# Kernel optimization log

Measured on AMD Instinct MI355X. Metric: run time of the kernel, lower is better.

Reference implementation:

```python
import jax, jax.numpy as jnp
import numpy as np

B, S, IN, D, H, K, NLVL = 8, 1536, 32, 128, 4, 7, 2
DFF = 4 * D
DK = D // H
EPS = 1e-6


def setup_inputs() -> dict:
    key = jax.random.key(0)
    ks = jax.random.split(key, 24)
    rn = lambda k, sh, s=0.05: jax.random.normal(k, sh, jnp.float32) * s
    z = lambda sh: jnp.zeros(sh, jnp.float32)
    o = lambda sh: jnp.ones(sh, jnp.float32)
    return {
        'x': jax.random.normal(ks[0], (B, S, IN), jnp.float32),
        'enc_W': rn(ks[1], (IN, D)), 'enc_b': z((D,)),
        'ln_rnn_a': o((NLVL, D)), 'ln_rnn_b': z((NLVL, D)),
        'gru_Wih': rn(ks[2], (NLVL, 3 * D, D)), 'gru_Whh': rn(ks[3], (NLVL, 3 * D, D)),
        'gru_bih': z((NLVL, 3 * D)), 'gru_bhh': z((NLVL, 3 * D)),
        'ln_attn_a': o((NLVL, D)), 'ln_attn_b': z((NLVL, D)),
        'Wq': rn(ks[4], (NLVL, D, D)), 'bq': z((NLVL, D)),
        'Wk': rn(ks[5], (NLVL, D, D)), 'bk': z((NLVL, D)),
        'Wv': rn(ks[6], (NLVL, D, D)), 'bv': z((NLVL, D)),
        'Wo': rn(ks[7], (NLVL, D, D)), 'bo': z((NLVL, D)),
        'ln_ff_a': o((NLVL, D)), 'ln_ff_b': z((NLVL, D)),
        'ff_W1': rn(ks[8], (NLVL, D, DFF)), 'ff_b1': z((NLVL, DFF)),
        'ff_W2': rn(ks[9], (NLVL, DFF, D)), 'ff_b2': z((NLVL, D)),
        'out_W': rn(ks[10], (D, 1)), 'out_b': z((1,)),
    }


def layernorm(x, a, b):
    # faithful to torch code: unbiased std (ddof=1), divide by (std + eps)
    m = x.mean(-1, keepdims=True)
    s = jnp.std(x, axis=-1, ddof=1, keepdims=True)
    return a * (x - m) / (s + EPS) + b


def local_rnn(x, Wih, Whh, bih, bhh):
    # x: [B,S,D]. Window each position into its ksize-length causal window,
    # run a GRU over the window (scan over K steps, batched over B*S), keep last h.
    xp = jnp.pad(x, ((0, 0), (K - 1, 0), (0, 0)))            # zero left-pad
    win = jnp.stack([xp[:, i:i + S] for i in range(K)], 0)   # [K,B,S,D]

    def step(h, xt):
        gi = xt @ Wih.T + bih                                 # [B,S,3D]
        gh = h @ Whh.T + bhh
        ir, iz, inn = jnp.split(gi, 3, -1)
        hr, hz, hn = jnp.split(gh, 3, -1)
        r = jax.nn.sigmoid(ir + hr)
        zz = jax.nn.sigmoid(iz + hz)
        nn_ = jnp.tanh(inn + r * hn)
        return (1.0 - zz) * nn_ + zz * h, None

    h, _ = jax.lax.scan(step, jnp.zeros_like(x), win)
    return h


def mhpool(x, Wq, bq, Wk, bk, Wv, bv, Wo, bo):
    def heads(w, bb):
        return jnp.swapaxes((x @ w + bb).reshape(B, S, H, DK), 1, 2)  # [B,H,S,DK]
    q, k, v = heads(Wq, bq), heads(Wk, bk), heads(Wv, bv)
    scores = jnp.einsum('bhqd,bhkd->bhqk', q, k) / np.float32(np.sqrt(DK))
    mask = jnp.tril(jnp.ones((S, S), bool))
    scores = jnp.where(mask, scores, jnp.float32(-1e9))
    p = jax.nn.softmax(scores, axis=-1)
    o = jnp.einsum('bhqk,bhkd->bhqd', p, v)
    o = jnp.swapaxes(o, 1, 2).reshape(B, S, D)
    return o @ Wo + bo


def reference(x, enc_W, enc_b, ln_rnn_a, ln_rnn_b, gru_Wih, gru_Whh, gru_bih,
              gru_bhh, ln_attn_a, ln_attn_b, Wq, bq, Wk, bk, Wv, bv, Wo, bo,
              ln_ff_a, ln_ff_b, ff_W1, ff_b1, ff_W2, ff_b2, out_W, out_b):
    h = x @ enc_W + enc_b
    for i in range(NLVL):
        # LocalRNNLayer (pre-norm residual); LocalRNN.output Linear is unused in orig forward
        h = h + local_rnn(layernorm(h, ln_rnn_a[i], ln_rnn_b[i]),
                          gru_Wih[i], gru_Whh[i], gru_bih[i], gru_bhh[i])
        # MHPooling sublayer
        h = h + mhpool(layernorm(h, ln_attn_a[i], ln_attn_b[i]),
                       Wq[i], bq[i], Wk[i], bk[i], Wv[i], bv[i], Wo[i], bo[i])
        # PositionwiseFeedForward sublayer
        hn = layernorm(h, ln_ff_a[i], ln_ff_b[i])
        h = h + (jax.nn.relu(hn @ ff_W1[i] + ff_b1[i]) @ ff_W2[i] + ff_b2[i])
    return jax.nn.sigmoid(h @ out_W + out_b)
```

## Files before the change

kernel.cpp:

```cpp
#include <hip/hip_runtime.h>
#include <math.h>

#define DEV_INLINE __device__ __forceinline__

constexpr int B = 8, S = 1536, IN = 32, D = 128, NH = 4, KWIN = 7, NLVL = 2;
constexpr int DFF = 512, DKH = 32;
constexpr int M = B * S;
constexpr int MD = M * D;
constexpr float EPS = 1e-6f;

typedef unsigned short u16;
typedef __bf16 bf16x8 __attribute__((ext_vector_type(8)));
typedef float f32x4 __attribute__((ext_vector_type(4)));
typedef unsigned short u16x4 __attribute__((ext_vector_type(4)));

#define MFMA16(a, b, c) __builtin_amdgcn_mfma_f32_16x16x32_bf16(a, b, c, 0, 0, 0)

DEV_INLINE float sigmoidf_(float x) { return 1.f / (1.f + __expf(-x)); }

DEV_INLINE u16 f2bf(float f) {
    unsigned u = __builtin_bit_cast(unsigned, f);
    unsigned rnd = 0x7FFFu + ((u >> 16) & 1u);
    return (u16)((u + rnd) >> 16);
}
// ... 59 lines not shown
        if (i < SZ_FF) {
            int lvl = i >> 16, rem = i & 65535, k = rem >> 7, n = rem & 127;
            W2T[(size_t)lvl * 65536 + n * 512 + k] = f2bf(W2[i]); return;
        }
        return;
    }
    const int row0 = (blockIdx.x - 2304) * 32;
    for (int i = tid; i < 32 * 32; i += 256) xs[i >> 5][i & 31] = x[(size_t)row0 * IN + i];
    for (int i = tid; i < 32 * 128; i += 256) Ws[i >> 7][i & 127] = encW[i];
    __syncthreads();
    const int r = tid >> 3, cg = (tid & 7) * 16;
    float acc[16];
    #pragma unroll
    for (int j = 0; j < 16; ++j) acc[j] = encb[cg + j];
    for (int k = 0; k < IN; ++k) {
        const float xv = xs[r][k];
        #pragma unroll
        for (int j = 0; j < 16; ++j) acc[j] = fmaf(xv, Ws[k][cg + j], acc[j]);
    }
    float s = 0.f;
    #pragma unroll
    for (int j = 0; j < 16; ++j) s += acc[j];
    s += __shfl_xor(s, 1); s += __shfl_xor(s, 2); s += __shfl_xor(s, 4);
    const float mean = s * (1.f / D);
    float q = 0.f;
    #pragma unroll
    for (int j = 0; j < 16; ++j) { float d = acc[j] - mean; q += d * d; }
    q += __shfl_xor(q, 1); q += __shfl_xor(q, 2); q += __shfl_xor(q, 4);
    const float inv = 1.f / (sqrtf(q * (1.f / (D - 1))) + EPS);
    float* hp = h + (size_t)(row0 + r) * D + cg;
    u16* xp = xnout + (size_t)(row0 + r) * D + cg;
    #pragma unroll
    for (int jj = 0; jj < 4; ++jj) {
        float4 hv = make_float4(acc[4 * jj], acc[4 * jj + 1], acc[4 * jj + 2], acc[4 * jj + 3]);
        *(float4*)(hp + 4 * jj) = hv;
        u16x4 o;
        #pragma unroll
        for (int c = 0; c < 4; ++c)
            o[c] = f2bf(ga[cg + 4 * jj + c] * (acc[4 * jj + c] - mean) * inv + gb[cg + 4 * jj + c]);
        *(u16x4*)(xp + 4 * jj) = o;
    }
}

__global__ __launch_bounds__(512, 2) void k_gru_qkv(
    const u16* __restrict__ xn,
    const u16* __restrict__ Wih16,
    const u16* __restrict__ Whh16,
    const float* __restrict__ bih, const float* __restrict__ bhh,
    float* __restrict__ hout,
    const float* __restrict__ ga, const float* __restrict__ gb,
    const u16* __restrict__ Wqkv,
    const float* __restrict__ bq, const float* __restrict__ bk, const float* __restrict__ bv,
    u16* __restrict__ q16, u16* __restrict__ k16, u16* __restrict__ vt16) {
    constexpr int RB = 48;
    constexpr float QS = 0.17677669529663687f * 1.4426950408889634f;
    __shared__ __align__(16) u16 xnS[64 * 136];
    __shared__ __align__(16) u16 Gs[64 * 392];
    __shared__ __align__(16) u16 hs16[RB * 136];
    const int tid = threadIdx.x;
    const int wave = tid >> 6, lane = tid & 63;
    const int col16 = lane & 15, quad = lane >> 4;
    const int row0 = blockIdx.x * RB;
    const int ss0 = row0 % S;
    const int cc = wave * 16 + col16;

    for (int i = tid; i < 64 * 16; i += 512) {
        const int r = i >> 4, c8 = (i & 15) * 8;
        bf16x8 val = {};
        if (ss0 - 16 + r >= 0)
            val = *(const bf16x8*)(xn + (size_t)(row0 - 16 + r) * 128 + c8);
        *(bf16x8*)&xnS[r * 136 + c8] = val;
    }
    bf16x8 Breg[3][4];
    #pragma unroll
    for (int g = 0; g < 3; ++g)
        #pragma unroll
        for (int kc = 0; kc < 4; ++kc)
            Breg[g][kc] = *(const bf16x8*)(Whh16 + (size_t)(g * 128 + cc) * 128 + kc * 32 + quad * 8);
    float bi[3], bh[3];
    #pragma unroll
    for (int g = 0; g < 3; ++g) { bi[g] = bih[g * 128 + cc]; bh[g] = bhh[g * 128 + cc]; }
    __syncthreads();

    #pragma unroll
    for (int tt = wave; tt < 24; tt += 8) {
        const int rt = tt / 12, ct = tt - rt * 12;
        const u16* bp = Wih16 + (size_t)(ct * 32 + col16) * 128 + quad * 8;
        f32x4 a00 = {0.f, 0.f, 0.f, 0.f}, a01 = a00, a10 = a00, a11 = a00;
        #pragma unroll
        for (int k0 = 0; k0 < 128; k0 += 32) {
            bf16x8 af0 = *(const bf16x8*)&xnS[(rt * 32 + col16) * 136 + k0 + quad * 8];
            bf16x8 af1 = *(const bf16x8*)&xnS[(rt * 32 + 16 + col16) * 136 + k0 + quad * 8];
            bf16x8 b0 = *(const bf16x8*)(bp + k0);
            bf16x8 b1 = *(const bf16x8*)(bp + 16 * 128 + k0);
            a00 = MFMA16(af0, b0, a00);
            a01 = MFMA16(af0, b1, a01);
            a10 = MFMA16(af1, b0, a10);
            a11 = MFMA16(af1, b1, a11);
        }
        #pragma unroll
        for (int r = 0; r < 4; ++r) {
            const int gr0 = rt * 32 + quad * 4 + r, gr1 = gr0 + 16;
            Gs[gr0 * 392 + ct * 32 + col16]      = f2bf(a00[r]);
            Gs[gr0 * 392 + ct * 32 + 16 + col16] = f2bf(a01[r]);
            Gs[gr1 * 392 + ct * 32 + col16]      = f2bf(a10[r]);
            Gs[gr1 * 392 + ct * 32 + 16 + col16] = f2bf(a11[r]);
        }
    }
    float hp[12] = {};
    __syncthreads();

    for (int t = 0; t < KWIN; ++t) {
        const int shift = KWIN - 1 - t;
        f32x4 acc[3][3];
        #pragma unroll
        for (int rh = 0; rh < 3; ++rh)
            #pragma unroll
            for (int g = 0; g < 3; ++g) acc[rh][g] = {0.f, 0.f, 0.f, 0.f};
        if (t > 0) {
            bf16x8 af[3][4];
            #pragma unroll
            for (int rh = 0; rh < 3; ++rh)
                #pragma unroll
                for (int kc = 0; kc < 4; ++kc)
                    af[rh][kc] = *(const bf16x8*)&hs16[(rh * 16 + col16) * 136 + kc * 32 + quad * 8];
            __syncthreads();
            #pragma unroll
            for (int kc = 0; kc < 4; ++kc)
                #pragma unroll
                for (int g = 0; g < 3; ++g)
                    #pragma unroll
                    for (int rh = 0; rh < 3; ++rh)
                        acc[rh][g] = MFMA16(af[rh][kc], Breg[g][kc], acc[rh][g]);
        }
        const bool last = (t == KWIN - 1);
        #pragma unroll
        for (int rh = 0; rh < 3; ++rh) {
            #pragma unroll
            for (int r = 0; r < 4; ++r) {
                const int idx = rh * 4 + r;
                const int lrow = rh * 16 + quad * 4 + r;
                const int gr = lrow - shift + 16;
                const float xr  = b2f(Gs[gr * 392 + cc]);
                const float xz  = b2f(Gs[gr * 392 + 128 + cc]);
                const float xn_ = b2f(Gs[gr * 392 + 256 + cc]);
                const float rr = sigmoidf_(xr + bi[0] + acc[rh][0][r] + bh[0]);
                const float zz = sigmoidf_(xz + bi[1] + acc[rh][1][r] + bh[1]);
                const float e2 = __expf(2.f * (xn_ + bi[2] + rr * (acc[rh][2][r] + bh[2])));
                const float nn = 1.f - 2.f / (e2 + 1.f);
                const float hnew = (1.f - zz) * nn + zz * hp[idx];
                hp[idx] = hnew;
                if (!last) hs16[lrow * 136 + cc] = f2bf(hnew);
            }
        }
        __syncthreads();
    }
    float* hf = (float*)Gs;
    #pragma unroll
    for (int rh = 0; rh < 3; ++rh)
        #pragma unroll
        for (int r = 0; r < 4; ++r) {
            const int lrow = rh * 16 + quad * 4 + r;
            const float hv = hp[rh * 4 + r] + hout[(size_t)(row0 + lrow) * D + cc];
            hout[(size_t)(row0 + lrow) * D + cc] = hv;
            hf[lrow * 132 + cc] = hv;
        }
    __syncthreads();
    {
        const int r = tid >> 3;
        if (r < RB) {
            const int cg = (tid & 7) * 16;
            float vals[16];
            #pragma unroll
            for (int jj = 0; jj < 4; ++jj) {
                float4 v = *(const float4*)&hf[r * 132 + cg + 4 * jj];
                vals[4 * jj] = v.x; vals[4 * jj + 1] = v.y; vals[4 * jj + 2] = v.z; vals[4 * jj + 3] = v.w;
            }
            float s = 0.f;
            #pragma unroll
            for (int j = 0; j < 16; ++j) s += vals[j];
            s += __shfl_xor(s, 1); s += __shfl_xor(s, 2); s += __shfl_xor(s, 4);
            const float mean = s * (1.f / D);
            float q = 0.f;
            #pragma unroll
            for (int j = 0; j < 16; ++j) { float d = vals[j] - mean; q += d * d; }
            q += __shfl_xor(q, 1); q += __shfl_xor(q, 2); q += __shfl_xor(q, 4);
            const float inv = 1.f / (sqrtf(q * (1.f / (D - 1))) + EPS);
            #pragma unroll
            for (int jj = 0; jj < 4; ++jj) {
                u16x4 o;
                #pragma unroll
                for (int c = 0; c < 4; ++c)
                    o[c] = f2bf(ga[cg + 4 * jj + c] * (vals[4 * jj + c] - mean) * inv + gb[cg + 4 * jj + c]);
                *(u16x4*)&hs16[r * 136 + cg + 4 * jj] = o;
            }
        }
    }
    __syncthreads();
    for (int tt = wave; tt < 36; tt += 8) {
        const int rt = tt / 12, ct = tt - rt * 12;
        const int seg = ct >> 2;
        const int c0 = (ct & 3) * 32;
        const u16* bp = Wqkv + (size_t)(seg * 128 + c0 + col16) * 128 + quad * 8;
        f32x4 a0 = {0.f, 0.f, 0.f, 0.f}, a1 = a0;
        #pragma unroll
        for (int k0 = 0; k0 < 128; k0 += 32) {
            bf16x8 af = *(const bf16x8*)&hs16[(rt * 16 + col16) * 136 + k0 + quad * 8];
            bf16x8 b0 = *(const bf16x8*)(bp + k0);
            bf16x8 b1 = *(const bf16x8*)(bp + 16 * 128 + k0);
            a0 = MFMA16(af, b0, a0);
            a1 = MFMA16(af, b1, a1);
        }
        if (seg < 2) {
            const float* bias = seg == 0 ? bq : bk;
            const float sc = seg == 0 ? QS : 1.f;
            const float bv0 = bias[c0 + col16], bv1 = bias[c0 + 16 + col16];
            u16* o16 = seg == 0 ? q16 : k16;
            #pragma unroll
            for (int r = 0; r < 4; ++r) {
                const size_t gr = (size_t)(row0 + rt * 16 + quad * 4 + r) * 128;
                o16[gr + c0 + col16]      = f2bf((a0[r] + bv0) * sc);
                o16[gr + c0 + 16 + col16] = f2bf((a1[r] + bv1) * sc);
            }
        } else {
            const float bv0 = bv[c0 + col16], bv1 = bv[c0 + 16 + col16];
            const int bb = row0 / S, ssv = row0 - bb * S + rt * 16;
            const int ca = c0 + col16, cb = c0 + 16 + col16;
            u16* pa = vt16 + ((size_t)((bb * NH + (ca >> 5)) * 32 + (ca & 31))) * S + ssv;
            u16* pb = vt16 + ((size_t)((bb * NH + (cb >> 5)) * 32 + (cb & 31))) * S + ssv;
            #pragma unroll
            for (int r = 0; r < 4; ++r) {
                pa[quad * 4 + r] = f2bf(a0[r] + bv0);
                pb[quad * 4 + r] = f2bf(a1[r] + bv1);
            }
        }
    }
}

__global__ __launch_bounds__(256) void k_attn_mfma(
    const u16* Qb, const u16* __restrict__ Kb,
    const u16* __restrict__ Vt, u16* O16) {
    const int wave = threadIdx.x >> 6, lane = threadIdx.x & 63;
    const int p = blockIdx.x;
    const int bh = blockIdx.y;
    const int b = bh >> 2, hh = bh & 3;
    const int col = lane & 15, quad = lane >> 4;

    __shared__ __align__(16) u16 Pb[4][32][40];
    __shared__ float Om[4][32][33];
    __shared__ float Lm[4][32];
    u16 (* __restrict__ P)[40] = Pb[wave];

    const u16* Kbase = Kb + (size_t)b * S * 128 + hh * 32;
    const u16* Vbase = Vt + (size_t)bh * 32 * S;

    #pragma unroll
    for (int half = 0; half < 2; ++half) {
        const int qt = half == 0 ? p : 47 - p;
        const int q0 = qt * 32;
        const int nkt = qt + 1;
        const u16* qp = Qb + (size_t)(b * S + q0 + col) * 128 + hh * 32 + quad * 8;
        const bf16x8 qf0 = *(const bf16x8*)qp;
        const bf16x8 qf1 = *(const bf16x8*)(qp + 16 * 128);
        f32x4 o00 = {0.f, 0.f, 0.f, 0.f}, o01 = o00, o10 = o00, o11 = o00;
        float lsum[8] = {};
        int kt = wave;
        bf16x8 kf0 = {}, kf1 = {}, vf0 = {}, vf1 = {};
        if (kt < nkt) {
            const u16* kp = Kbase + (size_t)(kt * 32 + col) * 128 + quad * 8;
            kf0 = *(const bf16x8*)kp;
            kf1 = *(const bf16x8*)(kp + 16 * 128);
            const u16* vp = Vbase + (size_t)col * S + kt * 32 + quad * 8;
            vf0 = *(const bf16x8*)vp;
            vf1 = *(const bf16x8*)(vp + 16 * S);
        }
        while (kt < nkt) {
            const int ktn = kt + 4;
            bf16x8 nk0 = kf0, nk1 = kf1, nv0 = vf0, nv1 = vf1;
            if (ktn < nkt) {
                const u16* kp = Kbase + (size_t)(ktn * 32 + col) * 128 + quad * 8;
                nk0 = *(const bf16x8*)kp;
                nk1 = *(const bf16x8*)(kp + 16 * 128);
                const u16* vp = Vbase + (size_t)col * S + ktn * 32 + quad * 8;
                nv0 = *(const bf16x8*)vp;
                nv1 = *(const bf16x8*)(vp + 16 * S);
            }
// ... 30 lines not shown
            o00 = MFMA16(pa0, vf0, o00);
            o01 = MFMA16(pa0, vf1, o01);
            o10 = MFMA16(pa1, vf0, o10);
            o11 = MFMA16(pa1, vf1, o11);
            kf0 = nk0; kf1 = nk1; vf0 = nv0; vf1 = nv1;
            kt = ktn;
        }
        #pragma unroll
        for (int i = 0; i < 8; ++i) {
            float v = lsum[i];
            v += __shfl_xor(v, 1); v += __shfl_xor(v, 2);
            v += __shfl_xor(v, 4); v += __shfl_xor(v, 8);
            lsum[i] = v;
        }
        #pragma unroll
        for (int r = 0; r < 4; ++r) {
            const int lr = quad * 4 + r;
            Om[wave][lr][col]           = o00[r];
            Om[wave][lr][16 + col]      = o01[r];
            Om[wave][16 + lr][col]      = o10[r];
            Om[wave][16 + lr][16 + col] = o11[r];
        }
        if (col == 0) {
            #pragma unroll
            for (int i = 0; i < 8; ++i)
                Lm[wave][(i >> 2) * 16 + quad * 4 + (i & 3)] = lsum[i];
        }
        __syncthreads();
        {
            const int tr = threadIdx.x >> 3, tc = (threadIdx.x & 7) * 4;
            const float inv = 1.f / (Lm[0][tr] + Lm[1][tr] + Lm[2][tr] + Lm[3][tr]);
            u16x4 outv;
            #pragma unroll
            for (int c = 0; c < 4; ++c) {
                const float o = Om[0][tr][tc + c] + Om[1][tr][tc + c] +
                                Om[2][tr][tc + c] + Om[3][tr][tc + c];
                outv[c] = f2bf(o * inv);
            }
            *(u16x4*)(O16 + (size_t)(b * S + q0 + tr) * 128 + hh * 32 + tc) = outv;
        }
        __syncthreads();
    }
}

template <bool LAST>
__global__ __launch_bounds__(256) void k_mho_ffn(
    const u16* __restrict__ ao, const u16* __restrict__ WoT, const float* __restrict__ bo,
    float* __restrict__ hio,
    const float* __restrict__ ga1, const float* __restrict__ gb1,
    const u16* __restrict__ W1T, const float* __restrict__ b1,
    const u16* __restrict__ W2T, const float* __restrict__ b2,
    const float* __restrict__ ga2, const float* __restrict__ gb2, u16* __restrict__ xnout,
    const float* __restrict__ outW, const float* __restrict__ outb, float* __restrict__ outp) {
    __shared__ float hL[32 * 132];
    __shared__ __align__(16) u16 xnL[32 * 136];
    __shared__ __align__(16) u16 Ls[32 * 520];
    const int tid = threadIdx.x;
    const int wave = tid >> 6, lane = tid & 63;
    const int col16 = lane & 15, quad = lane >> 4;
    const int row0 = blockIdx.x * 32;
    const int c0 = wave * 32;

    {
        const u16* a0p = ao + (size_t)(row0 + col16) * 128 + quad * 8;
        const u16* b0p = WoT + (size_t)(c0 + col16) * 128 + quad * 8;
        f32x4 acc00 = {0.f, 0.f, 0.f, 0.f}, acc01 = acc00, acc10 = acc00, acc11 = acc00;
        mfma_tile32<128>(a0p, a0p + 16 * 128, b0p, b0p + 16 * 128, acc00, acc01, acc10, acc11);
        const float bv0 = bo[c0 + col16];
        const float bv1 = bo[c0 + 16 + col16];
        #pragma unroll
        for (int r = 0; r < 4; ++r) {
            const int l0 = quad * 4 + r, l1 = 16 + quad * 4 + r;
            const size_t g0 = (size_t)(row0 + l0) * D, g1 = (size_t)(row0 + l1) * D;
            hL[l0 * 132 + c0 + col16]      = acc00[r] + bv0 + hio[g0 + c0 + col16];
            hL[l0 * 132 + c0 + 16 + col16] = acc01[r] + bv1 + hio[g0 + c0 + 16 + col16];
            hL[l1 * 132 + c0 + col16]      = acc10[r] + bv0 + hio[g1 + c0 + col16];
            hL[l1 * 132 + c0 + 16 + col16] = acc11[r] + bv1 + hio[g1 + c0 + 16 + col16];
        }
    }
    __syncthreads();
    {
        const int r = tid >> 3, cg = (tid & 7) * 16;
        float vals[16];
        #pragma unroll
        for (int jj = 0; jj < 4; ++jj) {
            float4 v = *(const float4*)&hL[r * 132 + cg + 4 * jj];
            vals[4 * jj] = v.x; vals[4 * jj + 1] = v.y; vals[4 * jj + 2] = v.z; vals[4 * jj + 3] = v.w;
        }
        float s = 0.f;
        #pragma unroll
        for (int j = 0; j < 16; ++j) s += vals[j];
        s += __shfl_xor(s, 1); s += __shfl_xor(s, 2); s += __shfl_xor(s, 4);
        const float mean = s * (1.f / D);
        float q = 0.f;
        #pragma unroll
        for (int j = 0; j < 16; ++j) { float d = vals[j] - mean; q += d * d; }
        q += __shfl_xor(q, 1); q += __shfl_xor(q, 2); q += __shfl_xor(q, 4);
        const float inv = 1.f / (sqrtf(q * (1.f / (D - 1))) + EPS);
        #pragma unroll
        for (int jj = 0; jj < 4; ++jj) {
            u16x4 o;
            #pragma unroll
            for (int c = 0; c < 4; ++c)
                o[c] = f2bf(ga1[cg + 4 * jj + c] * (vals[4 * jj + c] - mean) * inv + gb1[cg + 4 * jj + c]);
            *(u16x4*)&xnL[r * 136 + cg + 4 * jj] = o;
        }
    }
    __syncthreads();
    #pragma unroll
    for (int ct = 0; ct < 4; ++ct) {
        const int c0f = wave * 128 + ct * 32;
        const u16* b0p = W1T + (size_t)(c0f + col16) * 128 + quad * 8;
        f32x4 acc00 = {0.f, 0.f, 0.f, 0.f}, acc01 = acc00, acc10 = acc00, acc11 = acc00;
        #pragma unroll
        for (int k0 = 0; k0 < 128; k0 += 32) {
            bf16x8 a0 = *(const bf16x8*)&xnL[col16 * 136 + k0 + quad * 8];
            bf16x8 a1 = *(const bf16x8*)&xnL[(16 + col16) * 136 + k0 + quad * 8];
            bf16x8 b0 = *(const bf16x8*)(b0p + k0);
            bf16x8 b1 = *(const bf16x8*)(b0p + 16 * 128 + k0);
            acc00 = MFMA16(a0, b0, acc00);
            acc01 = MFMA16(a0, b1, acc01);
            acc10 = MFMA16(a1, b0, acc10);
            acc11 = MFMA16(a1, b1, acc11);
        }
        const float bv0 = b1[c0f + col16];
        const float bv1 = b1[c0f + 16 + col16];
        #pragma unroll
        for (int r = 0; r < 4; ++r) {
            const int l0 = quad * 4 + r, l1 = 16 + quad * 4 + r;
            Ls[l0 * 520 + c0f + col16]      = f2bf(fmaxf(acc00[r] + bv0, 0.f));
            Ls[l0 * 520 + c0f + 16 + col16] = f2bf(fmaxf(acc01[r] + bv1, 0.f));
            Ls[l1 * 520 + c0f + col16]      = f2bf(fmaxf(acc10[r] + bv0, 0.f));
            Ls[l1 * 520 + c0f + 16 + col16] = f2bf(fmaxf(acc11[r] + bv1, 0.f));
        }
    }
    __syncthreads();
    {
        f32x4 acc00 = {0.f, 0.f, 0.f, 0.f}, acc01 = acc00, acc10 = acc00, acc11 = acc00;
        #pragma unroll
        for (int k0 = 0; k0 < 512; k0 += 32) {
            bf16x8 a0 = *(const bf16x8*)&Ls[col16 * 520 + k0 + quad * 8];
            bf16x8 a1 = *(const bf16x8*)&Ls[(16 + col16) * 520 + k0 + quad * 8];
            const u16* bp = W2T + (size_t)(c0 + col16) * 512 + k0 + quad * 8;
            bf16x8 b0 = *(const bf16x8*)bp;
            bf16x8 b1v = *(const bf16x8*)(bp + 16 * 512);
            acc00 = MFMA16(a0, b0, acc00);
            acc01 = MFMA16(a0, b1v, acc01);
            acc10 = MFMA16(a1, b0, acc10);
            acc11 = MFMA16(a1, b1v, acc11);
        }
        const float bv0 = b2[c0 + col16];
        const float bv1 = b2[c0 + 16 + col16];
        #pragma unroll
        for (int r = 0; r < 4; ++r) {
            const int l0 = quad * 4 + r, l1 = 16 + quad * 4 + r;
            const size_t g0 = (size_t)(row0 + l0) * D, g1 = (size_t)(row0 + l1) * D;
            const float v00 = acc00[r] + bv0 + hL[l0 * 132 + c0 + col16];
            const float v01 = acc01[r] + bv1 + hL[l0 * 132 + c0 + 16 + col16];
            const float v10 = acc10[r] + bv0 + hL[l1 * 132 + c0 + col16];
            const float v11 = acc11[r] + bv1 + hL[l1 * 132 + c0 + 16 + col16];
            hio[g0 + c0 + col16]      = v00;
            hio[g0 + c0 + 16 + col16] = v01;
            hio[g1 + c0 + col16]      = v10;
            hio[g1 + c0 + 16 + col16] = v11;
            hL[l0 * 132 + c0 + col16]      = v00;
            hL[l0 * 132 + c0 + 16 + col16] = v01;
            hL[l1 * 132 + c0 + col16]      = v10;
            hL[l1 * 132 + c0 + 16 + col16] = v11;
        }
    }
    __syncthreads();
    {
        const int r = tid >> 3, cg = (tid & 7) * 16;
        float vals[16];
        #pragma unroll
        for (int jj = 0; jj < 4; ++jj) {
            float4 v = *(const float4*)&hL[r * 132 + cg + 4 * jj];
            vals[4 * jj] = v.x; vals[4 * jj + 1] = v.y; vals[4 * jj + 2] = v.z; vals[4 * jj + 3] = v.w;
        }
        if constexpr (LAST) {
            float dot = 0.f;
            #pragma unroll
            for (int j = 0; j < 16; ++j) dot += vals[j] * outW[cg + j];
            dot += __shfl_xor(dot, 1); dot += __shfl_xor(dot, 2); dot += __shfl_xor(dot, 4);
            if ((tid & 7) == 0) outp[row0 + r] = sigmoidf_(dot + outb[0]);
        } else {
            float s = 0.f;
            #pragma unroll
            for (int j = 0; j < 16; ++j) s += vals[j];
            s += __shfl_xor(s, 1); s += __shfl_xor(s, 2); s += __shfl_xor(s, 4);
            const float mean = s * (1.f / D);
            float q = 0.f;
            #pragma unroll
            for (int j = 0; j < 16; ++j) { float d = vals[j] - mean; q += d * d; }
            q += __shfl_xor(q, 1); q += __shfl_xor(q, 2); q += __shfl_xor(q, 4);
            const float inv = 1.f / (sqrtf(q * (1.f / (D - 1))) + EPS);
            u16* xp = xnout + (size_t)(row0 + r) * D + cg;
            #pragma unroll
            for (int jj = 0; jj < 4; ++jj) {
                u16x4 o;
                #pragma unroll
                for (int c = 0; c < 4; ++c)
                    o[c] = f2bf(ga2[cg + 4 * jj + c] * (vals[4 * jj + c] - mean) * inv + gb2[cg + 4 * jj + c]);
                *(u16x4*)(xp + 4 * jj) = o;
            }
        }
    }
}

extern "C" void kernel_launch(void* const* d_in, const int* in_sizes, int n_in,
                              void* d_out, int out_size, void* d_ws, size_t ws_size,
                              hipStream_t stream) {
    const float* x       = (const float*)d_in[0];
    const float* enc_W   = (const float*)d_in[1];
    const float* enc_b   = (const float*)d_in[2];
    const float* ln_rnn_a = (const float*)d_in[3];
    const float* ln_rnn_b = (const float*)d_in[4];
    const float* gru_Wih = (const float*)d_in[5];
    const float* gru_Whh = (const float*)d_in[6];
    const float* gru_bih = (const float*)d_in[7];
    const float* gru_bhh = (const float*)d_in[8];
    const float* ln_attn_a = (const float*)d_in[9];
    const float* ln_attn_b = (const float*)d_in[10];
    const float* Wq = (const float*)d_in[11];
    const float* bq = (const float*)d_in[12];
    const float* Wk = (const float*)d_in[13];
    const float* bk = (const float*)d_in[14];
    const float* Wv = (const float*)d_in[15];
    const float* bv = (const float*)d_in[16];
    const float* Wo = (const float*)d_in[17];
    const float* bo = (const float*)d_in[18];
    const float* ln_ff_a = (const float*)d_in[19];
    const float* ln_ff_b = (const float*)d_in[20];
    const float* ff_W1 = (const float*)d_in[21];
    const float* ff_b1 = (const float*)d_in[22];
    const float* ff_W2 = (const float*)d_in[23];
    const float* ff_b2 = (const float*)d_in[24];
    const float* out_W = (const float*)d_in[25];
    const float* out_b = (const float*)d_in[26];

    float* h   = (float*)d_ws;
    u16* pool  = (u16*)(h + MD);
    u16* xn16  = pool + (size_t)3 * MD;
    u16* Wih16 = xn16 + MD;
    u16* Whh16 = Wih16 + NLVL * 384 * D;
    u16* Wqkv  = Whh16 + NLVL * 384 * D;
    u16* WoT   = Wqkv + NLVL * 384 * D;
    u16* W1T   = WoT + NLVL * D * D;
    u16* W2T   = W1T + NLVL * D * DFF;

    u16* q16   = pool;
    u16* k16   = pool + MD;
    u16* vt16  = pool + (size_t)2 * MD;
    u16* ao16  = q16;

    k_prep_enc<<<2688, 256, 0, stream>>>(
        gru_Wih, gru_Whh, Wq, Wk, Wv, Wo, ff_W1, ff_W2,
        Wih16, Whh16, Wqkv, WoT, W1T, W2T,
        x, enc_W, enc_b, ln_rnn_a, ln_rnn_b, h, xn16);

    for (int lvl = 0; lvl < NLVL; ++lvl) {
        k_gru_qkv<<<256, 512, 0, stream>>>(
            xn16, Wih16 + lvl * 384 * D, Whh16 + lvl * 384 * D,
            gru_bih + lvl * 384, gru_bhh + lvl * 384,
            h, ln_attn_a + lvl * D, ln_attn_b + lvl * D,
            Wqkv + lvl * 384 * D, bq + lvl * D, bk + lvl * D, bv + lvl * D,
            q16, k16, vt16);

        k_attn_mfma<<<dim3(24, 32), 256, 0, stream>>>(q16, k16, vt16, ao16);

        if (lvl + 1 < NLVL) {
            k_mho_ffn<false><<<M / 32, 256, 0, stream>>>(
                ao16, WoT + lvl * D * D, bo + lvl * D, h,
                ln_ff_a + lvl * D, ln_ff_b + lvl * D,
                W1T + lvl * D * DFF, ff_b1 + lvl * DFF,
                W2T + lvl * DFF * D, ff_b2 + lvl * D,
                ln_rnn_a + (lvl + 1) * D, ln_rnn_b + (lvl + 1) * D, xn16,
                nullptr, nullptr, nullptr);
        } else {
            k_mho_ffn<true><<<M / 32, 256, 0, stream>>>(
                ao16, WoT + lvl * D * D, bo + lvl * D, h,
                ln_ff_a + lvl * D, ln_ff_b + lvl * D,
                W1T + lvl * D * DFF, ff_b1 + lvl * DFF,
                W2T + lvl * DFF * D, ff_b2 + lvl * D,
                nullptr, nullptr, nullptr,
                out_W, out_b, (float*)d_out);
        }
    }
}
```

Measured before the change: 320.0 us.

## Double-buffer GRU hidden state, trim halo, load x from global, halve FFN row tile

The GRU kernel no longer stages the normalized input in shared memory. The input projection reads its A operand directly from global, and the window halo shrinks from 16 rows to 6, so Gs shrinks to 54 rows. The hidden-state buffer is double-buffered, which removes one __syncthreads per recurrence step. Separately, the MHO/FFN kernel processes 16 rows per block instead of 32, doubling the grid and cutting shared memory and registers for occupancy, at the cost of reloading weights twice as often.

```diff
diff --git a/kernel.cpp b/kernel.cpp
--- a/kernel.cpp
+++ b/kernel.cpp
@@ -137,9 +137,9 @@
     u16* __restrict__ q16, u16* __restrict__ k16, u16* __restrict__ vt16) {
     constexpr int RB = 48;
     constexpr float QS = 0.17677669529663687f * 1.4426950408889634f;
-    __shared__ __align__(16) u16 xnS[64 * 136];
-    __shared__ __align__(16) u16 Gs[64 * 392];
-    __shared__ __align__(16) u16 hs16[RB * 136];
+    __shared__ __align__(16) u16 Gs[54 * 392];
+    __shared__ __align__(16) u16 hsA[RB * 136];
+    __shared__ __align__(16) u16 hsB[RB * 136];
     const int tid = threadIdx.x;
     const int wave = tid >> 6, lane = tid & 63;
     const int col16 = lane & 15, quad = lane >> 4;
@@ -147,13 +147,6 @@
     const int ss0 = row0 % S;
     const int cc = wave * 16 + col16;
 
-    for (int i = tid; i < 64 * 16; i += 512) {
-        const int r = i >> 4, c8 = (i & 15) * 8;
-        bf16x8 val = {};
-        if (ss0 - 16 + r >= 0)
-            val = *(const bf16x8*)(xn + (size_t)(row0 - 16 + r) * 128 + c8);
-        *(bf16x8*)&xnS[r * 136 + c8] = val;
-    }
     bf16x8 Breg[3][4];
     #pragma unroll
     for (int g = 0; g < 3; ++g)
@@ -163,17 +156,23 @@
     float bi[3], bh[3];
     #pragma unroll
     for (int g = 0; g < 3; ++g) { bi[g] = bih[g * 128 + cc]; bh[g] = bhh[g * 128 + cc]; }
-    __syncthreads();
 
     #pragma unroll
     for (int tt = wave; tt < 24; tt += 8) {
         const int rt = tt / 12, ct = tt - rt * 12;
+        const int gr0 = rt * 22;
+        const bool v0 = (ss0 - 6 + gr0 + col16) >= 0;
+        const int grow0 = row0 - 6 + gr0 + col16;
+        const int grow1 = grow0 + 16;
+        const u16* a0g = xn + (size_t)(v0 ? grow0 : row0) * 128 + quad * 8;
+        const u16* a1g = xn + (size_t)grow1 * 128 + quad * 8;
         const u16* bp = Wih16 + (size_t)(ct * 32 + col16) * 128 + quad * 8;
         f32x4 a00 = {0.f, 0.f, 0.f, 0.f}, a01 = a00, a10 = a00, a11 = a00;
         #pragma unroll
         for (int k0 = 0; k0 < 128; k0 += 32) {
-            bf16x8 af0 = *(const bf16x8*)&xnS[(rt * 32 + col16) * 136 + k0 + quad * 8];
-            bf16x8 af1 = *(const bf16x8*)&xnS[(rt * 32 + 16 + col16) * 136 + k0 + quad * 8];
+            bf16x8 af0 = *(const bf16x8*)(a0g + k0);
+            if (!v0) af0 = (bf16x8){};
+            bf16x8 af1 = *(const bf16x8*)(a1g + k0);
             bf16x8 b0 = *(const bf16x8*)(bp + k0);
             bf16x8 b1 = *(const bf16x8*)(bp + 16 * 128 + k0);
             a00 = MFMA16(af0, b0, a00);
@@ -183,11 +182,11 @@
         }
         #pragma unroll
         for (int r = 0; r < 4; ++r) {
-            const int gr0 = rt * 32 + quad * 4 + r, gr1 = gr0 + 16;
-            Gs[gr0 * 392 + ct * 32 + col16]      = f2bf(a00[r]);
-            Gs[gr0 * 392 + ct * 32 + 16 + col16] = f2bf(a01[r]);
-            Gs[gr1 * 392 + ct * 32 + col16]      = f2bf(a10[r]);
-            Gs[gr1 * 392 + ct * 32 + 16 + col16] = f2bf(a11[r]);
+            const int g0r = gr0 + quad * 4 + r, g1r = g0r + 16;
+            Gs[g0r * 392 + ct * 32 + col16]      = f2bf(a00[r]);
+            Gs[g0r * 392 + ct * 32 + 16 + col16] = f2bf(a01[r]);
+            Gs[g1r * 392 + ct * 32 + col16]      = f2bf(a10[r]);
+            Gs[g1r * 392 + ct * 32 + 16 + col16] = f2bf(a11[r]);
         }
     }
     float hp[12] = {};
@@ -195,6 +194,8 @@
 
     for (int t = 0; t < KWIN; ++t) {
         const int shift = KWIN - 1 - t;
+        u16* wbuf = (t & 1) ? hsB : hsA;
+        const u16* rbuf = (t & 1) ? hsA : hsB;
         f32x4 acc[3][3];
         #pragma unroll
         for (int rh = 0; rh < 3; ++rh)
@@ -206,8 +207,7 @@
             for (int rh = 0; rh < 3; ++rh)
                 #pragma unroll
                 for (int kc = 0; kc < 4; ++kc)
-                    af[rh][kc] = *(const bf16x8*)&hs16[(rh * 16 + col16) * 136 + kc * 32 + quad * 8];
-            __syncthreads();
+                    af[rh][kc] = *(const bf16x8*)&rbuf[(rh * 16 + col16) * 136 + kc * 32 + quad * 8];
             #pragma unroll
             for (int kc = 0; kc < 4; ++kc)
                 #pragma unroll
@@ -223,7 +223,7 @@
             for (int r = 0; r < 4; ++r) {
                 const int idx = rh * 4 + r;
                 const int lrow = rh * 16 + quad * 4 + r;
-                const int gr = lrow - shift + 16;
+                const int gr = lrow - shift + 6;
                 const float xr  = b2f(Gs[gr * 392 + cc]);
                 const float xz  = b2f(Gs[gr * 392 + 128 + cc]);
                 const float xn_ = b2f(Gs[gr * 392 + 256 + cc]);
@@ -233,7 +233,7 @@
                 const float nn = 1.f - 2.f / (e2 + 1.f);
                 const float hnew = (1.f - zz) * nn + zz * hp[idx];
                 hp[idx] = hnew;
-                if (!last) hs16[lrow * 136 + cc] = f2bf(hnew);
+                if (!last) wbuf[lrow * 136 + cc] = f2bf(hnew);
             }
         }
         __syncthreads();
@@ -275,7 +275,7 @@
                 #pragma unroll
                 for (int c = 0; c < 4; ++c)
                     o[c] = f2bf(ga[cg + 4 * jj + c] * (vals[4 * jj + c] - mean) * inv + gb[cg + 4 * jj + c]);
-                *(u16x4*)&hs16[r * 136 + cg + 4 * jj] = o;
+                *(u16x4*)&hsA[r * 136 + cg + 4 * jj] = o;
             }
         }
     }
@@ -288,7 +288,7 @@
         f32x4 a0 = {0.f, 0.f, 0.f, 0.f}, a1 = a0;
         #pragma unroll
         for (int k0 = 0; k0 < 128; k0 += 32) {
-            bf16x8 af = *(const bf16x8*)&hs16[(rt * 16 + col16) * 136 + k0 + quad * 8];
+            bf16x8 af = *(const bf16x8*)&hsA[(rt * 16 + col16) * 136 + k0 + quad * 8];
             bf16x8 b0 = *(const bf16x8*)(bp + k0);
             bf16x8 b1 = *(const bf16x8*)(bp + 16 * 128 + k0);
             a0 = MFMA16(af, b0, a0);
@@ -451,53 +451,58 @@
     const u16* __restrict__ W2T, const float* __restrict__ b2,
     const float* __restrict__ ga2, const float* __restrict__ gb2, u16* __restrict__ xnout,
     const float* __restrict__ outW, const float* __restrict__ outb, float* __restrict__ outp) {
-    __shared__ float hL[32 * 132];
-    __shared__ __align__(16) u16 xnL[32 * 136];
-    __shared__ __align__(16) u16 Ls[32 * 520];
+    __shared__ float hL[16 * 132];
+    __shared__ __align__(16) u16 xnL[16 * 136];
+    __shared__ __align__(16) u16 Ls[16 * 520];
     const int tid = threadIdx.x;
     const int wave = tid >> 6, lane = tid & 63;
     const int col16 = lane & 15, quad = lane >> 4;
-    const int row0 = blockIdx.x * 32;
+    const int row0 = blockIdx.x * 16;
     const int c0 = wave * 32;
 
     {
         const u16* a0p = ao + (size_t)(row0 + col16) * 128 + quad * 8;
         const u16* b0p = WoT + (size_t)(c0 + col16) * 128 + quad * 8;
-        f32x4 acc00 = {0.f, 0.f, 0.f, 0.f}, acc01 = acc00, acc10 = acc00, acc11 = acc00;
-        mfma_tile32<128>(a0p, a0p + 16 * 128, b0p, b0p + 16 * 128, acc00, acc01, acc10, acc11);
-        const float bv0 = bo[c0 + col16];
-        const float bv1 = bo[c0 + 16 + col16];
+        const u16* b1p = b0p + 16 * 128;
+        f32x4 acc0 = {0.f, 0.f, 0.f, 0.f}, acc1 = acc0;
+        #pragma unroll
+        for (int k0 = 0; k0 < 128; k0 += 32) {
+            bf16x8 a0 = *(const bf16x8*)(a0p + k0);
+            bf16x8 b0 = *(const bf16x8*)(b0p + k0);
+            bf16x8 b1 = *(const bf16x8*)(b1p + k0);
+            acc0 = MFMA16(a0, b0, acc0);
+            acc1 = MFMA16(a0, b1, acc1);
+        }
+        const float bv0 = bo[c0 + col16], bv1 = bo[c0 + 16 + col16];
         #pragma unroll
         for (int r = 0; r < 4; ++r) {
-            const int l0 = quad * 4 + r, l1 = 16 + quad * 4 + r;
-            const size_t g0 = (size_t)(row0 + l0) * D, g1 = (size_t)(row0 + l1) * D;
-            hL[l0 * 132 + c0 + col16]      = acc00[r] + bv0 + hio[g0 + c0 + col16];
-            hL[l0 * 132 + c0 + 16 + col16] = acc01[r] + bv1 + hio[g0 + c0 + 16 + col16];
-            hL[l1 * 132 + c0 + col16]      = acc10[r] + bv0 + hio[g1 + c0 + col16];
-            hL[l1 * 132 + c0 + 16 + col16] = acc11[r] + bv1 + hio[g1 + c0 + 16 + col16];
+            const int l0 = quad * 4 + r;
+            const size_t g0 = (size_t)(row0 + l0) * D;
+            hL[l0 * 132 + c0 + col16]      = acc0[r] + bv0 + hio[g0 + c0 + col16];
+            hL[l0 * 132 + c0 + 16 + col16] = acc1[r] + bv1 + hio[g0 + c0 + 16 + col16];
         }
     }
     __syncthreads();
     {
-        const int r = tid >> 3, cg = (tid & 7) * 16;
-        float vals[16];
-        #pragma unroll
-        for (int jj = 0; jj < 4; ++jj) {
+        const int r = tid >> 4, cg = (tid & 15) * 8;
+        float vals[8];
+        #pragma unroll
+        for (int jj = 0; jj < 2; ++jj) {
             float4 v = *(const float4*)&hL[r * 132 + cg + 4 * jj];
             vals[4 * jj] = v.x; vals[4 * jj + 1] = v.y; vals[4 * jj + 2] = v.z; vals[4 * jj + 3] = v.w;
         }
         float s = 0.f;
         #pragma unroll
-        for (int j = 0; j < 16; ++j) s += vals[j];
-        s += __shfl_xor(s, 1); s += __shfl_xor(s, 2); s += __shfl_xor(s, 4);
+        for (int j = 0; j < 8; ++j) s += vals[j];
+        s += __shfl_xor(s, 1); s += __shfl_xor(s, 2); s += __shfl_xor(s, 4); s += __shfl_xor(s, 8);
         const float mean = s * (1.f / D);
         float q = 0.f;
         #pragma unroll
-        for (int j = 0; j < 16; ++j) { float d = vals[j] - mean; q += d * d; }
-        q += __shfl_xor(q, 1); q += __shfl_xor(q, 2); q += __shfl_xor(q, 4);
+        for (int j = 0; j < 8; ++j) { float d = vals[j] - mean; q += d * d; }
+        q += __shfl_xor(q, 1); q += __shfl_xor(q, 2); q += __shfl_xor(q, 4); q += __shfl_xor(q, 8);
         const float inv = 1.f / (sqrtf(q * (1.f / (D - 1))) + EPS);
         #pragma unroll
-        for (int jj = 0; jj < 4; ++jj) {
+        for (int jj = 0; jj < 2; ++jj) {
             u16x4 o;
             #pragma unroll
             for (int c = 0; c < 4; ++c)
@@ -510,93 +515,79 @@
     for (int ct = 0; ct < 4; ++ct) {
         const int c0f = wave * 128 + ct * 32;
         const u16* b0p = W1T + (size_t)(c0f + col16) * 128 + quad * 8;
-        f32x4 acc00 = {0.f, 0.f, 0.f, 0.f}, acc01 = acc00, acc10 = acc00, acc11 = acc00;
+        const u16* b1p = b0p + 16 * 128;
+        f32x4 acc0 = {0.f, 0.f, 0.f, 0.f}, acc1 = acc0;
         #pragma unroll
         for (int k0 = 0; k0 < 128; k0 += 32) {
             bf16x8 a0 = *(const bf16x8*)&xnL[col16 * 136 + k0 + quad * 8];
-            bf16x8 a1 = *(const bf16x8*)&xnL[(16 + col16) * 136 + k0 + quad * 8];
             bf16x8 b0 = *(const bf16x8*)(b0p + k0);
-            bf16x8 b1 = *(const bf16x8*)(b0p + 16 * 128 + k0);
-            acc00 = MFMA16(a0, b0, acc00);
-            acc01 = MFMA16(a0, b1, acc01);
-            acc10 = MFMA16(a1, b0, acc10);
-            acc11 = MFMA16(a1, b1, acc11);
-        }
-        const float bv0 = b1[c0f + col16];
-        const float bv1 = b1[c0f + 16 + col16];
+            bf16x8 b1 = *(const bf16x8*)(b1p + k0);
+            acc0 = MFMA16(a0, b0, acc0);
+            acc1 = MFMA16(a0, b1, acc1);
+        }
+        const float bv0 = b1[c0f + col16], bv1 = b1[c0f + 16 + col16];
         #pragma unroll
         for (int r = 0; r < 4; ++r) {
-            const int l0 = quad * 4 + r, l1 = 16 + quad * 4 + r;
-            Ls[l0 * 520 + c0f + col16]      = f2bf(fmaxf(acc00[r] + bv0, 0.f));
-            Ls[l0 * 520 + c0f + 16 + col16] = f2bf(fmaxf(acc01[r] + bv1, 0.f));
-            Ls[l1 * 520 + c0f + col16]      = f2bf(fmaxf(acc10[r] + bv0, 0.f));
-            Ls[l1 * 520 + c0f + 16 + col16] = f2bf(fmaxf(acc11[r] + bv1, 0.f));
+            const int l0 = quad * 4 + r;
+            Ls[l0 * 520 + c0f + col16]      = f2bf(fmaxf(acc0[r] + bv0, 0.f));
+            Ls[l0 * 520 + c0f + 16 + col16] = f2bf(fmaxf(acc1[r] + bv1, 0.f));
         }
     }
     __syncthreads();
     {
-        f32x4 acc00 = {0.f, 0.f, 0.f, 0.f}, acc01 = acc00, acc10 = acc00, acc11 = acc00;
+        f32x4 acc0 = {0.f, 0.f, 0.f, 0.f}, acc1 = acc0;
         #pragma unroll
         for (int k0 = 0; k0 < 512; k0 += 32) {
             bf16x8 a0 = *(const bf16x8*)&Ls[col16 * 520 + k0 + quad * 8];
-            bf16x8 a1 = *(const bf16x8*)&Ls[(16 + col16) * 520 + k0 + quad * 8];
             const u16* bp = W2T + (size_t)(c0 + col16) * 512 + k0 + quad * 8;
             bf16x8 b0 = *(const bf16x8*)bp;
             bf16x8 b1v = *(const bf16x8*)(bp + 16 * 512);
-            acc00 = MFMA16(a0, b0, acc00);
-            acc01 = MFMA16(a0, b1v, acc01);
-            acc10 = MFMA16(a1, b0, acc10);
-            acc11 = MFMA16(a1, b1v, acc11);
-        }
-        const float bv0 = b2[c0 + col16];
-        const float bv1 = b2[c0 + 16 + col16];
+            acc0 = MFMA16(a0, b0, acc0);
+            acc1 = MFMA16(a0, b1v, acc1);
+        }
+        const float bv0 = b2[c0 + col16], bv1 = b2[c0 + 16 + col16];
         #pragma unroll
         for (int r = 0; r < 4; ++r) {
-            const int l0 = quad * 4 + r, l1 = 16 + quad * 4 + r;
-            const size_t g0 = (size_t)(row0 + l0) * D, g1 = (size_t)(row0 + l1) * D;
-            const float v00 = acc00[r] + bv0 + hL[l0 * 132 + c0 + col16];
-            const float v01 = acc01[r] + bv1 + hL[l0 * 132 + c0 + 16 + col16];
-            const float v10 = acc10[r] + bv0 + hL[l1 * 132 + c0 + col16];
-            const float v11 = acc11[r] + bv1 + hL[l1 * 132 + c0 + 16 + col16];
-            hio[g0 + c0 + col16]      = v00;
-            hio[g0 + c0 + 16 + col16] = v01;
-            hio[g1 + c0 + col16]      = v10;
-            hio[g1 + c0 + 16 + col16] = v11;
-            hL[l0 * 132 + c0 + col16]      = v00;
-            hL[l0 * 132 + c0 + 16 + col16] = v01;
-            hL[l1 * 132 + c0 + col16]      = v10;
-            hL[l1 * 132 + c0 + 16 + col16] = v11;
+            const int l0 = quad * 4 + r;
+            const size_t g0 = (size_t)(row0 + l0) * D;
+            const float v0 = acc0[r] + bv0 + hL[l0 * 132 + c0 + col16];
+            const float v1 = acc1[r] + bv1 + hL[l0 * 132 + c0 + 16 + col16];
+            hio[g0 + c0 + col16]      = v0;
+            hio[g0 + c0 + 16 + col16] = v1;
+            hL[l0 * 132 + c0 + col16]      = v0;
+            hL[l0 * 132 + c0 + 16 + col16] = v1;
         }
     }
     __syncthreads();
     {
-        const int r = tid >> 3, cg = (tid & 7) * 16;
-        float vals[16];
-        #pragma unroll
-        for (int jj = 0; jj < 4; ++jj) {
+        const int r = tid >> 4, cg = (tid & 15) * 8;
+        float vals[8];
+        #pragma unroll
+        for (int jj = 0; jj < 2; ++jj) {
             float4 v = *(const float4*)&hL[r * 132 + cg + 4 * jj];
             vals[4 * jj] = v.x; vals[4 * jj + 1] = v.y; vals[4 * jj + 2] = v.z; vals[4 * jj + 3] = v.w;
         }
         if constexpr (LAST) {
             float dot = 0.f;
             #pragma unroll
-            for (int j = 0; j < 16; ++j) dot += vals[j] * outW[cg + j];
-            dot += __shfl_xor(dot, 1); dot += __shfl_xor(dot, 2); dot += __shfl_xor(dot, 4);
-            if ((tid & 7) == 0) outp[row0 + r] = sigmoidf_(dot + outb[0]);
+            for (int j = 0; j < 8; ++j) dot += vals[j] * outW[cg + j];
+            dot += __shfl_xor(dot, 1); dot += __shfl_xor(dot, 2);
+            dot += __shfl_xor(dot, 4); dot += __shfl_xor(dot, 8);
+            if ((tid & 15) == 0) outp[row0 + r] = sigmoidf_(dot + outb[0]);
         } else {
             float s = 0.f;
             #pragma unroll
-            for (int j = 0; j < 16; ++j) s += vals[j];
-            s += __shfl_xor(s, 1); s += __shfl_xor(s, 2); s += __shfl_xor(s, 4);
+            for (int j = 0; j < 8; ++j) s += vals[j];
+            s += __shfl_xor(s, 1); s += __shfl_xor(s, 2); s += __shfl_xor(s, 4); s += __shfl_xor(s, 8);
             const float mean = s * (1.f / D);
             float q = 0.f;
             #pragma unroll
-            for (int j = 0; j < 16; ++j) { float d = vals[j] - mean; q += d * d; }
-            q += __shfl_xor(q, 1); q += __shfl_xor(q, 2); q += __shfl_xor(q, 4);
+            for (int j = 0; j < 8; ++j) { float d = vals[j] - mean; q += d * d; }
+            q += __shfl_xor(q, 1); q += __shfl_xor(q, 2); q += __shfl_xor(q, 4); q += __shfl_xor(q, 8);
             const float inv = 1.f / (sqrtf(q * (1.f / (D - 1))) + EPS);
             u16* xp = xnout + (size_t)(row0 + r) * D + cg;
             #pragma unroll
-            for (int jj = 0; jj < 4; ++jj) {
+            for (int jj = 0; jj < 2; ++jj) {
                 u16x4 o;
                 #pragma unroll
                 for (int c = 0; c < 4; ++c)
@@ -669,7 +660,7 @@
         k_attn_mfma<<<dim3(24, 32), 256, 0, stream>>>(q16, k16, vt16, ao16);
 
         if (lvl + 1 < NLVL) {
-            k_mho_ffn<false><<<M / 32, 256, 0, stream>>>(
+            k_mho_ffn<false><<<M / 16, 256, 0, stream>>>(
                 ao16, WoT + lvl * D * D, bo + lvl * D, h,
                 ln_ff_a + lvl * D, ln_ff_b + lvl * D,
                 W1T + lvl * D * DFF, ff_b1 + lvl * DFF,
@@ -677,7 +668,7 @@
                 ln_rnn_a + (lvl + 1) * D, ln_rnn_b + (lvl + 1) * D, xn16,
                 nullptr, nullptr, nullptr);
         } else {
-            k_mho_ffn<true><<<M / 32, 256, 0, stream>>>(
+            k_mho_ffn<true><<<M / 16, 256, 0, stream>>>(
                 ao16, WoT + lvl * D * D, bo + lvl * D, h,
                 ln_ff_a + lvl * D, ln_ff_b + lvl * D,
                 W1T + lvl * D * DFF, ff_b1 + lvl * DFF,
```

Result: slower. 334.6 us (+4.6%).

## Halve GRU row block to 24 rows and double-buffer hidden-state LDS

Applied to the files above, without the earlier changes.

The fused GRU+QKV kernel now handles 24 output rows per block instead of 48, with an 8-row halo instead of 16. This raises the grid from 256 to 512 blocks so more blocks are resident across the CUs. The hidden-state LDS buffer is split into two ping-pong buffers, which removes one __syncthreads per recurrence step. In exchange, MFMA tiles are padded to 32 rows with 8 rows masked out, so about a quarter of the matrix work is wasted. Halo recompute per output row also goes up.

```diff
diff --git a/kernel.cpp b/kernel.cpp
--- a/kernel.cpp
+++ b/kernel.cpp
@@ -135,11 +135,12 @@
     const u16* __restrict__ Wqkv,
     const float* __restrict__ bq, const float* __restrict__ bk, const float* __restrict__ bv,
     u16* __restrict__ q16, u16* __restrict__ k16, u16* __restrict__ vt16) {
-    constexpr int RB = 48;
+    constexpr int RB = 24;
     constexpr float QS = 0.17677669529663687f * 1.4426950408889634f;
-    __shared__ __align__(16) u16 xnS[64 * 136];
-    __shared__ __align__(16) u16 Gs[64 * 392];
-    __shared__ __align__(16) u16 hs16[RB * 136];
+    __shared__ __align__(16) u16 xnS[32 * 136];
+    __shared__ __align__(16) u16 Gs[32 * 392];
+    __shared__ __align__(16) u16 hsA[32 * 136];
+    __shared__ __align__(16) u16 hsB[32 * 136];
     const int tid = threadIdx.x;
     const int wave = tid >> 6, lane = tid & 63;
     const int col16 = lane & 15, quad = lane >> 4;
@@ -147,11 +148,11 @@
     const int ss0 = row0 % S;
     const int cc = wave * 16 + col16;
 
-    for (int i = tid; i < 64 * 16; i += 512) {
-        const int r = i >> 4, c8 = (i & 15) * 8;
+    {
+        const int r = tid >> 4, c8 = (tid & 15) * 8;
         bf16x8 val = {};
-        if (ss0 - 16 + r >= 0)
-            val = *(const bf16x8*)(xn + (size_t)(row0 - 16 + r) * 128 + c8);
+        if (ss0 - 8 + r >= 0)
+            val = *(const bf16x8*)(xn + (size_t)(row0 - 8 + r) * 128 + c8);
         *(bf16x8*)&xnS[r * 136 + c8] = val;
     }
     bf16x8 Breg[3][4];
@@ -169,84 +170,84 @@
     for (int tt = wave; tt < 24; tt += 8) {
         const int rt = tt / 12, ct = tt - rt * 12;
         const u16* bp = Wih16 + (size_t)(ct * 32 + col16) * 128 + quad * 8;
-        f32x4 a00 = {0.f, 0.f, 0.f, 0.f}, a01 = a00, a10 = a00, a11 = a00;
+        f32x4 a0 = {0.f, 0.f, 0.f, 0.f}, a1 = a0;
         #pragma unroll
         for (int k0 = 0; k0 < 128; k0 += 32) {
-            bf16x8 af0 = *(const bf16x8*)&xnS[(rt * 32 + col16) * 136 + k0 + quad * 8];
-            bf16x8 af1 = *(const bf16x8*)&xnS[(rt * 32 + 16 + col16) * 136 + k0 + quad * 8];
+            bf16x8 af = *(const bf16x8*)&xnS[(rt * 16 + col16) * 136 + k0 + quad * 8];
             bf16x8 b0 = *(const bf16x8*)(bp + k0);
             bf16x8 b1 = *(const bf16x8*)(bp + 16 * 128 + k0);
-            a00 = MFMA16(af0, b0, a00);
-            a01 = MFMA16(af0, b1, a01);
-            a10 = MFMA16(af1, b0, a10);
-            a11 = MFMA16(af1, b1, a11);
+            a0 = MFMA16(af, b0, a0);
+            a1 = MFMA16(af, b1, a1);
         }
         #pragma unroll
         for (int r = 0; r < 4; ++r) {
-            const int gr0 = rt * 32 + quad * 4 + r, gr1 = gr0 + 16;
-            Gs[gr0 * 392 + ct * 32 + col16]      = f2bf(a00[r]);
-            Gs[gr0 * 392 + ct * 32 + 16 + col16] = f2bf(a01[r]);
-            Gs[gr1 * 392 + ct * 32 + col16]      = f2bf(a10[r]);
-            Gs[gr1 * 392 + ct * 32 + 16 + col16] = f2bf(a11[r]);
-        }
-    }
-    float hp[12] = {};
+            const int gr = rt * 16 + quad * 4 + r;
+            Gs[gr * 392 + ct * 32 + col16]      = f2bf(a0[r]);
+            Gs[gr * 392 + ct * 32 + 16 + col16] = f2bf(a1[r]);
+        }
+    }
+    float hp[8] = {};
     __syncthreads();
 
     for (int t = 0; t < KWIN; ++t) {
         const int shift = KWIN - 1 - t;
-        f32x4 acc[3][3];
-        #pragma unroll
-        for (int rh = 0; rh < 3; ++rh)
+        u16* wbuf = (t & 1) ? hsB : hsA;
+        const u16* rbuf = (t & 1) ? hsA : hsB;
+        f32x4 acc[2][3];
+        #pragma unroll
+        for (int rh = 0; rh < 2; ++rh)
             #pragma unroll
             for (int g = 0; g < 3; ++g) acc[rh][g] = {0.f, 0.f, 0.f, 0.f};
         if (t > 0) {
-            bf16x8 af[3][4];
-            #pragma unroll
-            for (int rh = 0; rh < 3; ++rh)
+            bf16x8 af[2][4];
+            #pragma unroll
+            for (int rh = 0; rh < 2; ++rh)
                 #pragma unroll
                 for (int kc = 0; kc < 4; ++kc)
-                    af[rh][kc] = *(const bf16x8*)&hs16[(rh * 16 + col16) * 136 + kc * 32 + quad * 8];
-            __syncthreads();
+                    af[rh][kc] = *(const bf16x8*)&rbuf[(rh * 16 + col16) * 136 + kc * 32 + quad * 8];
             #pragma unroll
             for (int kc = 0; kc < 4; ++kc)
                 #pragma unroll
                 for (int g = 0; g < 3; ++g)
                     #pragma unroll
-                    for (int rh = 0; rh < 3; ++rh)
+                    for (int rh = 0; rh < 2; ++rh)
                         acc[rh][g] = MFMA16(af[rh][kc], Breg[g][kc], acc[rh][g]);
         }
         const bool last = (t == KWIN - 1);
         #pragma unroll
-        for (int rh = 0; rh < 3; ++rh) {
+        for (int rh = 0; rh < 2; ++rh) {
             #pragma unroll
             for (int r = 0; r < 4; ++r) {
-                const int idx = rh * 4 + r;
                 const int lrow = rh * 16 + quad * 4 + r;
-                const int gr = lrow - shift + 16;
-                const float xr  = b2f(Gs[gr * 392 + cc]);
-                const float xz  = b2f(Gs[gr * 392 + 128 + cc]);
-                const float xn_ = b2f(Gs[gr * 392 + 256 + cc]);
-                const float rr = sigmoidf_(xr + bi[0] + acc[rh][0][r] + bh[0]);
-                const float zz = sigmoidf_(xz + bi[1] + acc[rh][1][r] + bh[1]);
-                const float e2 = __expf(2.f * (xn_ + bi[2] + rr * (acc[rh][2][r] + bh[2])));
-                const float nn = 1.f - 2.f / (e2 + 1.f);
-                const float hnew = (1.f - zz) * nn + zz * hp[idx];
-                hp[idx] = hnew;
-                if (!last) hs16[lrow * 136 + cc] = f2bf(hnew);
+                if (lrow < RB) {
+                    const int idx = rh * 4 + r;
+                    const int gr = lrow - shift + 8;
+                    const float xr  = b2f(Gs[gr * 392 + cc]);
+                    const float xz  = b2f(Gs[gr * 392 + 128 + cc]);
+                    const float xn_ = b2f(Gs[gr * 392 + 256 + cc]);
+                    const float rr = sigmoidf_(xr + bi[0] + acc[rh][0][r] + bh[0]);
+                    const float zz = sigmoidf_(xz + bi[1] + acc[rh][1][r] + bh[1]);
+                    const float e2 = __expf(2.f * (xn_ + bi[2] + rr * (acc[rh][2][r] + bh[2])));
+                    const float nn = 1.f - 2.f / (e2 + 1.f);
+                    const float hnew = (1.f - zz) * nn + zz * hp[idx];
+                    hp[idx] = hnew;
+                    if (!last) wbuf[lrow * 136 + cc] = f2bf(hnew);
+                }
             }
         }
         __syncthreads();
     }
     float* hf = (float*)Gs;
     #pragma unroll
-    for (int rh = 0; rh < 3; ++rh)
+    for (int rh = 0; rh < 2; ++rh)
         #pragma unroll
         for (int r = 0; r < 4; ++r) {
             const int lrow = rh * 16 + quad * 4 + r;
-            const float hv = hp[rh * 4 + r] + hout[(size_t)(row0 + lrow) * D + cc];
-            hout[(size_t)(row0 + lrow) * D + cc] = hv;
-            hf[lrow * 132 + cc] = hv;
+            if (lrow < RB) {
+                const float hv = hp[rh * 4 + r] + hout[(size_t)(row0 + lrow) * D + cc];
+                hout[(size_t)(row0 + lrow) * D + cc] = hv;
+                hf[lrow * 132 + cc] = hv;
+            }
         }
     __syncthreads();
     {
@@ -275,12 +276,13 @@
                 #pragma unroll
                 for (int c = 0; c < 4; ++c)
                     o[c] = f2bf(ga[cg + 4 * jj + c] * (vals[4 * jj + c] - mean) * inv + gb[cg + 4 * jj + c]);
-                *(u16x4*)&hs16[r * 136 + cg + 4 * jj] = o;
-            }
-        }
-    }
-    __syncthreads();
-    for (int tt = wave; tt < 36; tt += 8) {
+                *(u16x4*)&hsA[r * 136 + cg + 4 * jj] = o;
+            }
+        }
+    }
+    __syncthreads();
+    #pragma unroll
+    for (int tt = wave; tt < 24; tt += 8) {
         const int rt = tt / 12, ct = tt - rt * 12;
         const int seg = ct >> 2;
         const int c0 = (ct & 3) * 32;
@@ -288,7 +290,7 @@
         f32x4 a0 = {0.f, 0.f, 0.f, 0.f}, a1 = a0;
         #pragma unroll
         for (int k0 = 0; k0 < 128; k0 += 32) {
-            bf16x8 af = *(const bf16x8*)&hs16[(rt * 16 + col16) * 136 + k0 + quad * 8];
+            bf16x8 af = *(const bf16x8*)&hsA[(rt * 16 + col16) * 136 + k0 + quad * 8];
             bf16x8 b0 = *(const bf16x8*)(bp + k0);
             bf16x8 b1 = *(const bf16x8*)(bp + 16 * 128 + k0);
             a0 = MFMA16(af, b0, a0);
@@ -301,20 +303,26 @@
             u16* o16 = seg == 0 ? q16 : k16;
             #pragma unroll
             for (int r = 0; r < 4; ++r) {
-                const size_t gr = (size_t)(row0 + rt * 16 + quad * 4 + r) * 128;
-                o16[gr + c0 + col16]      = f2bf((a0[r] + bv0) * sc);
-                o16[gr + c0 + 16 + col16] = f2bf((a1[r] + bv1) * sc);
+                const int lr = rt * 16 + quad * 4 + r;
+                if (lr < RB) {
+                    const size_t gr = (size_t)(row0 + lr) * 128;
+                    o16[gr + c0 + col16]      = f2bf((a0[r] + bv0) * sc);
+                    o16[gr + c0 + 16 + col16] = f2bf((a1[r] + bv1) * sc);
+                }
             }
         } else {
             const float bv0 = bv[c0 + col16], bv1 = bv[c0 + 16 + col16];
-            const int bb = row0 / S, ssv = row0 - bb * S + rt * 16;
+            const int bb = row0 / S, ssv = row0 - bb * S;
             const int ca = c0 + col16, cb = c0 + 16 + col16;
             u16* pa = vt16 + ((size_t)((bb * NH + (ca >> 5)) * 32 + (ca & 31))) * S + ssv;
             u16* pb = vt16 + ((size_t)((bb * NH + (cb >> 5)) * 32 + (cb & 31))) * S + ssv;
             #pragma unroll
             for (int r = 0; r < 4; ++r) {
-                pa[quad * 4 + r] = f2bf(a0[r] + bv0);
-                pb[quad * 4 + r] = f2bf(a1[r] + bv1);
+                const int lr = rt * 16 + quad * 4 + r;
+                if (lr < RB) {
+                    pa[lr] = f2bf(a0[r] + bv0);
+                    pb[lr] = f2bf(a1[r] + bv1);
+                }
             }
         }
     }
@@ -659,7 +667,7 @@
         x, enc_W, enc_b, ln_rnn_a, ln_rnn_b, h, xn16);
 
     for (int lvl = 0; lvl < NLVL; ++lvl) {
-        k_gru_qkv<<<256, 512, 0, stream>>>(
+        k_gru_qkv<<<M / 24, 512, 0, stream>>>(
             xn16, Wih16 + lvl * 384 * D, Whh16 + lvl * 384 * D,
             gru_bih + lvl * 384, gru_bhh + lvl * 384,
             h, ln_attn_a + lvl * D, ln_attn_b + lvl * D,
```

Result: slower. 332.5 us (+3.9%).
